# Kernel tuning notes

Measured on AMD Instinct MI355X. Metric: run time of the kernel, lower is better.

The kernel has to match this reference:

```python
import jax, jax.numpy as jnp
import numpy as np

B, S, H = 8, 2048, 1024

def setup_inputs() -> dict:
    key = jax.random.key(0)
    k1, k2, k3, k4, k5, k6 = jax.random.split(key, 6)
    scale = 1.0 / np.sqrt(H)
    return {
        "hidden_states": jax.random.normal(k1, (B, S, H), dtype=jnp.float32),
        "key_padding_mask": jax.random.bernoulli(k2, 0.1, (B, S)),  # True = padded key
        "Wq_w": jax.random.normal(k3, (H, H), dtype=jnp.float32) * scale,
        "Wq_b": jax.random.normal(k4, (H,), dtype=jnp.float32) * 0.01,
        "Wk_w": jax.random.normal(k5, (H, H), dtype=jnp.float32) * scale,
        "Wk_b": jax.random.normal(k6, (H,), dtype=jnp.float32) * 0.01,
    }

def reference(hidden_states, key_padding_mask, Wq_w, Wq_b, Wk_w, Wk_b):
    # torch nn.Linear: y = x @ W.T + b
    q = jnp.einsum("bsh,oh->bso", hidden_states, Wq_w) + Wq_b
    k = jnp.einsum("bsh,oh->bso", hidden_states, Wk_w) + Wk_b
    d = q.shape[-1]
    scores = jnp.einsum("bqd,bkd->bqk", q, k) / jnp.sqrt(jnp.asarray(d, q.dtype))
    # scores[mask] -= inf  -> masked key columns become -inf
    scores = jnp.where(key_padding_mask[:, None, :], -jnp.inf, scores)
    attn = jax.nn.softmax(scores, axis=2)  # [B, S, S]
    out = jnp.einsum("bqk,bkd->bqd", attn, hidden_states)  # values = hidden_states (no proj)
    return out
```

## Files before the change

kernel.cpp:

```cpp
#include <hip/hip_runtime.h>
#include <hip/hip_bf16.h>

using bf16 = __hip_bfloat16;

using frag_ab = __attribute__((ext_vector_type(8))) short;
using frag_cd = __attribute__((ext_vector_type(4))) float;

__device__ __forceinline__ unsigned short f2bu(float f) {
    bf16 h = __float2bfloat16(f);
    return *(unsigned short*)&h;
}

__device__ __forceinline__ void st_c(float* p, float v) { *p = v; }
__device__ __forceinline__ void st_c(bf16* p, float v)  { *p = __float2bfloat16(v); }

__device__ __forceinline__ void load16(const bf16* g, bf16* l) {
    __builtin_amdgcn_global_load_lds(
        (const __attribute__((address_space(1))) unsigned int*)g,
        (__attribute__((address_space(3))) unsigned int*)l,
        16, 0, 0);
}

template <typename TC, bool HAS_BIAS, bool MASK>
__global__ __launch_bounds__(512, 2)
void gemm8p(const bf16* __restrict__ A, const bf16* __restrict__ B,
            const float* __restrict__ bias, const int* __restrict__ mask,
            TC* __restrict__ C, int K, int lda, int ldb, int ldc,
            long sA, long sB, long sC, long sM, float scale)
{
    __shared__ short lds[65536];

    const int bz = blockIdx.z;
    const bf16* Ab = A + (long)bz * sA;
    const bf16* Bb = B + (long)bz * sB;
    TC* Cb = C + (long)bz * sC;
    const int* maskb = MASK ? (mask + (long)bz * sM) : nullptr;

    const int t    = threadIdx.x;
    const int wid  = t >> 6;
    const int lane = t & 63;
    const int m0 = blockIdx.x * 256;
    const int n0 = blockIdx.y * 256;
    const int wr = wid >> 2;
    const int wc = wid & 3;
    const int lrow = lane & 15;
    const int quad = lane >> 4;

    const int rco   = ((quad + ((lrow >> 1) & 3)) & 3) * 8;
    const int a_off = wr * 4096 + lrow * 32 + rco;
    const int b_off = wc * 2048 + lrow * 32 + rco;

    const int srow = wid * 32 + (lane >> 2);
    const int gk   = (((lane & 3) - (lane >> 3)) & 3) * 8;
    const bf16* srcA0 = Ab + (long)(m0 + srow) * lda + gk;
    const bf16* srcA1 = Ab + (long)(m0 + srow + 16) * lda + gk;
    const bf16* srcB0 = Bb + (long)(n0 + srow) * ldb + gk;
    const bf16* srcB1 = Bb + (long)(n0 + srow + 16) * ldb + gk;
    const int dst0 = wid * 1024 + lane * 8;

    frag_cd acc[8][4] = {};

#define STG(SLOT, PART, K0)                                                     \
    do {                                                                        \
        load16((PART ? srcB0 : srcA0) + (K0),                                   \
               (bf16*)&lds[(SLOT) * 16384 + (PART) * 8192 + dst0]);             \
        load16((PART ? srcB1 : srcA1) + (K0),                                   \
               (bf16*)&lds[(SLOT) * 16384 + (PART) * 8192 + dst0 + 512]);       \
    } while (0)

#define PHASE(SLOT, QM, DO_STG, SSLOT, SPART, SK0, VMN)                         \
    do {                                                                        \
        frag_ab af_[4], bf_[4];                                                 \
        _Pragma("unroll")                                                       \
        for (int i_ = 0; i_ < 4; ++i_)                                          \
            af_[i_] = *(const frag_ab*)&lds[(SLOT) * 16384 + a_off +            \
                                            (QM) * 2048 + i_ * 512];            \
        _Pragma("unroll")                                                       \
        for (int j_ = 0; j_ < 4; ++j_)                                          \
            bf_[j_] = *(const frag_ab*)&lds[(SLOT) * 16384 + 8192 + b_off +     \
                                            j_ * 512];                          \
        if (DO_STG) STG(SSLOT, SPART, SK0);                                     \
        __builtin_amdgcn_sched_barrier(0);                                      \
        __builtin_amdgcn_s_barrier();                                           \
        asm volatile("s_waitcnt lgkmcnt(0)" ::: "memory");                      \
        __builtin_amdgcn_sched_barrier(0);                                      \
        __builtin_amdgcn_s_setprio(1);                                          \
        _Pragma("unroll")                                                       \
        for (int i_ = 0; i_ < 4; ++i_)                                          \
            _Pragma("unroll")                                                   \
            for (int j_ = 0; j_ < 4; ++j_)                                      \
                acc[(QM) * 4 + i_][j_] = __builtin_amdgcn_mfma_f32_16x16x32_bf16( \
                    af_[i_], bf_[j_], acc[(QM) * 4 + i_][j_], 0, 0, 0);         \
        __builtin_amdgcn_s_setprio(0);                                          \
        __builtin_amdgcn_sched_barrier(0);                                      \
        if ((VMN) == 8) asm volatile("s_waitcnt vmcnt(8)" ::: "memory");        \
        else if ((VMN) == 4) asm volatile("s_waitcnt vmcnt(4)" ::: "memory");   \
        else if ((VMN) == 0) asm volatile("s_waitcnt vmcnt(0)" ::: "memory");   \
        __builtin_amdgcn_sched_barrier(0);                                      \
        __builtin_amdgcn_s_barrier();                                           \
    } while (0)

    STG(0, 0, 0);  STG(0, 1, 0);
    STG(1, 0, 32); STG(1, 1, 32);
    STG(2, 0, 64); STG(2, 1, 64);
    asm volatile("s_waitcnt vmcnt(8)" ::: "memory");
    __builtin_amdgcn_sched_barrier(0);
    __builtin_amdgcn_s_barrier();
    __builtin_amdgcn_sched_barrier(0);

    const int NI = K >> 7;
    for (int it = 0; it < NI - 1; ++it) {
        const int kb = it << 7;
        PHASE(0, 0, 1, 3, 0, kb + 96,  -1);
        PHASE(0, 1, 1, 3, 1, kb + 96,   8);
        PHASE(1, 0, 1, 0, 0, kb + 128, -1);
        PHASE(1, 1, 1, 0, 1, kb + 128,  8);
        PHASE(2, 0, 1, 1, 0, kb + 160, -1);
        PHASE(2, 1, 1, 1, 1, kb + 160,  8);
        PHASE(3, 0, 1, 2, 0, kb + 192, -1);
        PHASE(3, 1, 1, 2, 1, kb + 192,  8);
    }
    {
        const int kb = (NI - 1) << 7;
        PHASE(0, 0, 1, 3, 0, kb + 96, -1);
        PHASE(0, 1, 1, 3, 1, kb + 96,  8);
        PHASE(1, 0, 0, 0, 0, 0, -1);
        PHASE(1, 1, 0, 0, 0, 0,  4);
        PHASE(2, 0, 0, 0, 0, 0, -1);
        PHASE(2, 1, 0, 0, 0, 0,  0);
        PHASE(3, 0, 0, 0, 0, 0, -1);
        PHASE(3, 1, 0, 0, 0, 0, -1);
    }
#undef PHASE
#undef STG

#pragma unroll
    for (int j = 0; j < 4; ++j) {
        const int col = n0 + wc * 64 + j * 16 + lrow;
        const float bv = HAS_BIAS ? bias[col] : 0.0f;
        const bool msk = MASK ? (maskb[col] != 0) : false;
#pragma unroll
        for (int ai = 0; ai < 8; ++ai) {
            const int rbase = m0 + wr * 128 + ai * 16 + quad * 4;
#pragma unroll
            for (int r = 0; r < 4; ++r) {
                float v = acc[ai][j][r] * scale + bv;
                if (MASK && msk) v = -INFINITY;
                st_c(&Cb[(long)(rbase + r) * ldc + col], v);
            }
        }
    }
}

__global__ __launch_bounds__(256)
void convert_transpose(const float* __restrict__ X, bf16* __restrict__ Xb,
                       bf16* __restrict__ XT, int S, int H)
{
    __shared__ unsigned short tile[64][72];
    const int b = blockIdx.z;
    const float* Xp = X + (long)b * S * H;
    bf16* Xbp = Xb + (long)b * S * H;
    bf16* XTp = XT + (long)b * H * S;
    const int h0 = blockIdx.x * 64, s0 = blockIdx.y * 64;
    const int t = threadIdx.x;
    const int r  = t >> 4;
    const int c4 = (t & 15) * 4;

#pragma unroll
    for (int p = 0; p < 4; ++p) {
        const int row = r + p * 16;
        const float4 v = *(const float4*)&Xp[(long)(s0 + row) * H + h0 + c4];
        ushort4 u;
        u.x = f2bu(v.x); u.y = f2bu(v.y); u.z = f2bu(v.z); u.w = f2bu(v.w);
        *(ushort4*)&tile[row][c4] = u;
        *(ushort4*)&Xbp[(long)(s0 + row) * H + h0 + c4] = u;
    }
    __syncthreads();
#pragma unroll
    for (int p = 0; p < 4; ++p) {
        const int hrow = r + p * 16;
        ushort4 u;
        u.x = tile[c4 + 0][hrow];
        u.y = tile[c4 + 1][hrow];
        u.z = tile[c4 + 2][hrow];
        u.w = tile[c4 + 3][hrow];
        *(ushort4*)&XTp[(long)(h0 + hrow) * S + s0 + c4] = u;
    }
}

__global__ __launch_bounds__(256)
void convert_w2(const float* __restrict__ wa, const float* __restrict__ wb,
                bf16* __restrict__ out, int n4each)
{
    const int i = blockIdx.x * 256 + threadIdx.x;
    const bool second = i >= n4each;
    const float* src = second ? wb : wa;
    const int j = second ? i - n4each : i;
    const float4 v = ((const float4*)src)[j];
    ushort4 u;
    u.x = f2bu(v.x); u.y = f2bu(v.y); u.z = f2bu(v.z); u.w = f2bu(v.w);
    ((ushort4*)out)[i] = u;
}

__global__ __launch_bounds__(256)
void pack_bias(const float* __restrict__ qb, const float* __restrict__ kb,
               float* __restrict__ out, int H)
{
    const int i = blockIdx.x * 256 + threadIdx.x;
    out[i] = (i < H) ? qb[i] : kb[i - H];
}

__global__ __launch_bounds__(256)
void softmax_kernel(bf16* __restrict__ Smat, int Slen)
{
    const int row = blockIdx.x;
    bf16* srow = Smat + (long)row * Slen;

    const int t    = threadIdx.x;
    const int lane = t & 63;
    const int wid  = t >> 6;

    ushort4 u0 = ((const ushort4*)srow)[t * 2];
    ushort4 u1 = ((const ushort4*)srow)[t * 2 + 1];

    float vals[8];
    {
        const unsigned short us[8] = {u0.x, u0.y, u0.z, u0.w, u1.x, u1.y, u1.z, u1.w};
#pragma unroll
        for (int i = 0; i < 8; ++i) {
            unsigned int w = (unsigned int)us[i] << 16;
            vals[i] = *(float*)&w;
        }
    }

    float mx = vals[0];
#pragma unroll
    for (int i = 1; i < 8; ++i) mx = fmaxf(mx, vals[i]);

    __shared__ float red[4];
#pragma unroll
    for (int o = 32; o > 0; o >>= 1) mx = fmaxf(mx, __shfl_xor(mx, o, 64));
    if (lane == 0) red[wid] = mx;
    __syncthreads();
    mx = fmaxf(fmaxf(red[0], red[1]), fmaxf(red[2], red[3]));
    __syncthreads();

    float sum = 0.0f;
#pragma unroll
    for (int i = 0; i < 8; ++i) {
        const float e = __expf(vals[i] - mx);
        vals[i] = e;
        sum += e;
    }
#pragma unroll
    for (int o = 32; o > 0; o >>= 1) sum += __shfl_xor(sum, o, 64);
    if (lane == 0) red[wid] = sum;
    __syncthreads();
    sum = red[0] + red[1] + red[2] + red[3];

    const float inv = 1.0f / sum;
    ushort4 o0, o1;
    o0.x = f2bu(vals[0] * inv); o0.y = f2bu(vals[1] * inv);
    o0.z = f2bu(vals[2] * inv); o0.w = f2bu(vals[3] * inv);
    o1.x = f2bu(vals[4] * inv); o1.y = f2bu(vals[5] * inv);
    o1.z = f2bu(vals[6] * inv); o1.w = f2bu(vals[7] * inv);
    ((ushort4*)srow)[t * 2]     = o0;
    ((ushort4*)srow)[t * 2 + 1] = o1;
}

extern "C" void kernel_launch(void* const* d_in, const int* in_sizes, int n_in,
                              void* d_out, int out_size, void* d_ws, size_t ws_size,
                              hipStream_t stream)
{
    const float* hidden = (const float*)d_in[0];
    const int*   mask   = (const int*)d_in[1];
    const float* Wq_w   = (const float*)d_in[2];
    const float* Wq_b   = (const float*)d_in[3];
    const float* Wk_w   = (const float*)d_in[4];
    const float* Wk_b   = (const float*)d_in[5];
    float* out = (float*)d_out;

    const int B = 8, S = 2048, H = 1024;
    const int M = B * S;
    const long MH = (long)M * H;

    bf16* QK  = (bf16*)d_ws;
    bf16* XbT = QK + MH * 2;
    bf16* Sb  = XbT + MH;
    bf16* Xb  = Sb;
    bf16* Wb  = Xb + MH;
    float* biasP = (float*)(Wb + 2L * H * H);

    const dim3 blk(256);
    const dim3 blk512(512);

    convert_transpose<<<dim3(H / 64, S / 64, B), blk, 0, stream>>>(hidden, Xb, XbT, S, H);
    convert_w2<<<dim3(2 * H * H / 1024), blk, 0, stream>>>(Wq_w, Wk_w, Wb, H * H / 4);
    pack_bias<<<dim3(2 * H / 256), blk, 0, stream>>>(Wq_b, Wk_b, biasP, H);

    gemm8p<bf16, true, false><<<dim3(M / 256, 2 * H / 256, 1), blk512, 0, stream>>>(
        Xb, Wb, biasP, nullptr, QK, H, H, H, 2 * H, 0, 0, 0, 0, 1.0f);

    gemm8p<bf16, false, true><<<dim3(S / 256, S / 256, B), blk512, 0, stream>>>(
        QK, QK + H, nullptr, mask, Sb, H, 2 * H, 2 * H, S,
        (long)S * 2 * H, (long)S * 2 * H, (long)S * S, S, 1.0f / 32.0f);

    softmax_kernel<<<dim3(B * S), blk, 0, stream>>>(Sb, S);

    gemm8p<float, false, false><<<dim3(S / 256, H / 256, B), blk512, 0, stream>>>(
        Sb, XbT, nullptr, nullptr, out, S, S, S, H,
        (long)S * S, (long)H * S, (long)S * H, 0, 1.0f);
}
```

Before: 393.0 us.

## Double-buffer LDS fragment registers to overlap LDS reads with MFMA

Restructures the GEMM inner loop so the A/B fragments for the next phase are read from LDS into a second register set while the current phase's MFMAs run. It drops the per-phase barrier and lgkmcnt wait that sat between fragment loads and compute, leaving one barrier per phase, and retunes the vmcnt waits to match. This aims to hide LDS read latency behind matrix math. In exchange it raises VGPR pressure under the 512-thread, 2-blocks launch bound and relies on the compiler inserting the right lgkmcnt waits before fragments are used.

```diff
diff --git a/kernel.cpp b/kernel.cpp
--- a/kernel.cpp
+++ b/kernel.cpp
@@ -59,6 +59,7 @@
     const int dst0 = wid * 1024 + lane * 8;
 
     frag_cd acc[8][4] = {};
+    frag_ab A0[4], A1[4], B0[4], B1[4];
 
 #define STG(SLOT, PART, K0)                                                     \
     do {                                                                        \
@@ -68,36 +69,52 @@
                (bf16*)&lds[(SLOT) * 16384 + (PART) * 8192 + dst0 + 512]);       \
     } while (0)
 
-#define PHASE(SLOT, QM, DO_STG, SSLOT, SPART, SK0, VMN)                         \
-    do {                                                                        \
-        frag_ab af_[4], bf_[4];                                                 \
+#define LOADA(DST, SLOT, QM)                                                    \
+    do {                                                                        \
         _Pragma("unroll")                                                       \
         for (int i_ = 0; i_ < 4; ++i_)                                          \
-            af_[i_] = *(const frag_ab*)&lds[(SLOT) * 16384 + a_off +            \
+            DST[i_] = *(const frag_ab*)&lds[(SLOT) * 16384 + a_off +            \
                                             (QM) * 2048 + i_ * 512];            \
+    } while (0)
+
+#define LOADB(DST, SLOT)                                                        \
+    do {                                                                        \
         _Pragma("unroll")                                                       \
         for (int j_ = 0; j_ < 4; ++j_)                                          \
-            bf_[j_] = *(const frag_ab*)&lds[(SLOT) * 16384 + 8192 + b_off +     \
+            DST[j_] = *(const frag_ab*)&lds[(SLOT) * 16384 + 8192 + b_off +     \
                                             j_ * 512];                          \
-        if (DO_STG) STG(SSLOT, SPART, SK0);                                     \
-        __builtin_amdgcn_sched_barrier(0);                                      \
-        __builtin_amdgcn_s_barrier();                                           \
-        asm volatile("s_waitcnt lgkmcnt(0)" ::: "memory");                      \
-        __builtin_amdgcn_sched_barrier(0);                                      \
-        __builtin_amdgcn_s_setprio(1);                                          \
+    } while (0)
+
+#define MFMA16(AR, BR, QM)                                                      \
+    do {                                                                        \
         _Pragma("unroll")                                                       \
         for (int i_ = 0; i_ < 4; ++i_)                                          \
             _Pragma("unroll")                                                   \
             for (int j_ = 0; j_ < 4; ++j_)                                      \
                 acc[(QM) * 4 + i_][j_] = __builtin_amdgcn_mfma_f32_16x16x32_bf16( \
-                    af_[i_], bf_[j_], acc[(QM) * 4 + i_][j_], 0, 0, 0);         \
+                    AR[i_], BR[j_], acc[(QM) * 4 + i_][j_], 0, 0, 0);           \
+    } while (0)
+
+#define VMW(N)                                                                  \
+    do {                                                                        \
+        if ((N) == 6)      asm volatile("s_waitcnt vmcnt(6)" ::: "memory");     \
+        else if ((N) == 4) asm volatile("s_waitcnt vmcnt(4)" ::: "memory");     \
+        else if ((N) == 0) asm volatile("s_waitcnt vmcnt(0)" ::: "memory");     \
+    } while (0)
+
+#define PH(AR, BR, QM, ISSUE, NSLOT, NAR, NBR, NQM, DO_STG, SSLOT, SPART, SK0, VMN) \
+    do {                                                                        \
+        if ((ISSUE) >= 1) LOADA(NAR, NSLOT, NQM);                               \
+        if ((ISSUE) == 2) LOADB(NBR, NSLOT);                                    \
+        if (DO_STG) STG(SSLOT, SPART, SK0);                                     \
+        __builtin_amdgcn_sched_barrier(0);                                      \
+        __builtin_amdgcn_s_setprio(1);                                          \
+        MFMA16(AR, BR, QM);                                                     \
         __builtin_amdgcn_s_setprio(0);                                          \
         __builtin_amdgcn_sched_barrier(0);                                      \
-        if ((VMN) == 8) asm volatile("s_waitcnt vmcnt(8)" ::: "memory");        \
-        else if ((VMN) == 4) asm volatile("s_waitcnt vmcnt(4)" ::: "memory");   \
-        else if ((VMN) == 0) asm volatile("s_waitcnt vmcnt(0)" ::: "memory");   \
+        VMW(VMN);                                                               \
+        __builtin_amdgcn_s_barrier();                                           \
         __builtin_amdgcn_sched_barrier(0);                                      \
-        __builtin_amdgcn_s_barrier();                                           \
     } while (0)
 
     STG(0, 0, 0);  STG(0, 1, 0);
@@ -107,31 +124,37 @@
     __builtin_amdgcn_sched_barrier(0);
     __builtin_amdgcn_s_barrier();
     __builtin_amdgcn_sched_barrier(0);
+    LOADA(A0, 0, 0);
+    LOADB(B0, 0);
 
     const int NI = K >> 7;
     for (int it = 0; it < NI - 1; ++it) {
         const int kb = it << 7;
-        PHASE(0, 0, 1, 3, 0, kb + 96,  -1);
-        PHASE(0, 1, 1, 3, 1, kb + 96,   8);
-        PHASE(1, 0, 1, 0, 0, kb + 128, -1);
-        PHASE(1, 1, 1, 0, 1, kb + 128,  8);
-        PHASE(2, 0, 1, 1, 0, kb + 160, -1);
-        PHASE(2, 1, 1, 1, 1, kb + 160,  8);
-        PHASE(3, 0, 1, 2, 0, kb + 192, -1);
-        PHASE(3, 1, 1, 2, 1, kb + 192,  8);
+        PH(A0, B0, 0, 1, 0, A1, B1, 1, 1, 3, 0, kb + 96,   6);
+        PH(A1, B0, 1, 2, 1, A0, B1, 0, 1, 3, 1, kb + 96,  -1);
+        PH(A0, B1, 0, 1, 1, A1, B0, 1, 1, 0, 0, kb + 128,  6);
+        PH(A1, B1, 1, 2, 2, A0, B0, 0, 1, 0, 1, kb + 128, -1);
+        PH(A0, B0, 0, 1, 2, A1, B1, 1, 1, 1, 0, kb + 160,  6);
+        PH(A1, B0, 1, 2, 3, A0, B1, 0, 1, 1, 1, kb + 160, -1);
+        PH(A0, B1, 0, 1, 3, A1, B0, 1, 1, 2, 0, kb + 192,  6);
+        PH(A1, B1, 1, 2, 0, A0, B0, 0, 1, 2, 1, kb + 192, -1);
     }
     {
         const int kb = (NI - 1) << 7;
-        PHASE(0, 0, 1, 3, 0, kb + 96, -1);
-        PHASE(0, 1, 1, 3, 1, kb + 96,  8);
-        PHASE(1, 0, 0, 0, 0, 0, -1);
-        PHASE(1, 1, 0, 0, 0, 0,  4);
-        PHASE(2, 0, 0, 0, 0, 0, -1);
-        PHASE(2, 1, 0, 0, 0, 0,  0);
-        PHASE(3, 0, 0, 0, 0, 0, -1);
-        PHASE(3, 1, 0, 0, 0, 0, -1);
-    }
-#undef PHASE
+        PH(A0, B0, 0, 1, 0, A1, B1, 1, 1, 3, 0, kb + 96,   6);
+        PH(A1, B0, 1, 2, 1, A0, B1, 0, 1, 3, 1, kb + 96,  -1);
+        PH(A0, B1, 0, 1, 1, A1, B0, 1, 0, 0, 0, 0,         4);
+        PH(A1, B1, 1, 2, 2, A0, B0, 0, 0, 0, 0, 0,        -1);
+        PH(A0, B0, 0, 1, 2, A1, B1, 1, 0, 0, 0, 0,         0);
+        PH(A1, B0, 1, 2, 3, A0, B1, 0, 0, 0, 0, 0,        -1);
+        PH(A0, B1, 0, 1, 3, A1, B0, 1, 0, 0, 0, 0,        -1);
+        PH(A1, B1, 1, 0, 0, A0, B0, 0, 0, 0, 0, 0,        -1);
+    }
+#undef PH
+#undef VMW
+#undef MFMA16
+#undef LOADB
+#undef LOADA
 #undef STG
 
 #pragma unroll
```

New measurement: 380.4 us, median of 2. -3.2%, faster.
